# Performance work log

Hardware: AMD Instinct MI355X
Metric: run time of the kernel (lower is better)

Reference implementation:

```python
import jax, jax.numpy as jnp
import numpy as np

N, E, G = 50000, 800000, 128
IN, H, OUT = 64, 108, 108
EPS = 1e-12  # F.normalize eps


def _linear_params(key, fin, fout):
    s = 1.0 / np.sqrt(fin)
    kw, kb = jax.random.split(key)
    W = jax.random.uniform(kw, (fin, fout), jnp.float32, -s, s)
    b = jax.random.uniform(kb, (fout,), jnp.float32, -s, s)
    return W, b


def setup_inputs() -> dict:
    key = jax.random.key(0)
    ks = jax.random.split(key, 12)
    nodes_feat = jax.random.normal(ks[0], (N, IN), jnp.float32)
    edges_feat = jax.random.normal(ks[1], (E, 1), jnp.float32)
    nodes_num_norm_sqrt = jax.random.uniform(ks[2], (N,), jnp.float32)
    edges_num_norm_sqrt = jax.random.uniform(ks[3], (E,), jnp.float32)
    edges_src = jax.random.randint(ks[4], (E,), 0, N, jnp.int32)
    edges_dst = jax.random.randint(ks[5], (E,), 0, N, jnp.int32)
    graph_ids = jnp.sort(jax.random.randint(ks[6], (N,), 0, G, jnp.int32))
    W_emb, b_emb = _linear_params(ks[7], IN, H)
    Wp1, bp1 = _linear_params(ks[8], H, H)      # meanpool MLP, layer 1
    Wn1, bn1 = _linear_params(ks[9], 2 * H, H)  # node-apply, layer 1
    Wp2, bp2 = _linear_params(ks[10], H, H)     # meanpool MLP, output layer
    Wn2, bn2 = _linear_params(ks[11], 2 * H, OUT)
    return dict(nodes_feat=nodes_feat, edges_feat=edges_feat,
                nodes_num_norm_sqrt=nodes_num_norm_sqrt,
                edges_num_norm_sqrt=edges_num_norm_sqrt,
                edges_src=edges_src, edges_dst=edges_dst, graph_ids=graph_ids,
                W_emb=W_emb, b_emb=b_emb, Wp1=Wp1, bp1=bp1, Wn1=Wn1, bn1=bn1,
                Wp2=Wp2, bp2=bp2, Wn2=Wn2, bn2=bn2)


def _sage_layer(h, src, dst, Wp, bp, Wn, bn):
    # GraphSageLayer(meanpool, residual=True, dropout=0): 
    #  m_e = relu(Linear(h_src)); c_v = mean_{e->v} m_e; 
    #  h' = relu(L2norm(Linear([h, c]))); out = h_in + h'
    h_in = h
    m = jax.nn.relu(h @ Wp + bp)                       # pool MLP on nodes, then gather == per-edge MLP
    msg = m[src]                                       # [E, d]
    agg = jax.ops.segment_sum(msg, dst, num_segments=h.shape[0])
    deg = jax.ops.segment_sum(jnp.ones((msg.shape[0],), m.dtype), dst, num_segments=h.shape[0])
    c = agg / jnp.maximum(deg, 1.0)[:, None]           # mean reducer; 0 for isolated nodes
    bundle = jnp.concatenate([h, c], axis=1) @ Wn + bn
    nrm = jnp.linalg.norm(bundle, axis=1, keepdims=True)
    bundle = bundle / jnp.maximum(nrm, EPS)            # F.normalize(p=2, dim=1)
    return h_in + jax.nn.relu(bundle)


def reference(nodes_feat, edges_feat, nodes_num_norm_sqrt, edges_num_norm_sqrt,
              edges_src, edges_dst, graph_ids,
              W_emb, b_emb, Wp1, bp1, Wn1, bn1, Wp2, bp2, Wn2, bn2):
    h = nodes_feat @ W_emb + b_emb                      # embedding_h
    h = _sage_layer(h, edges_src, edges_dst, Wp1, bp1, Wn1, bn1)
    h = _sage_layer(h, edges_src, edges_dst, Wp2, bp2, Wn2, bn2)
    # dgl.mean_nodes: per-graph mean of node features
    s = jax.ops.segment_sum(h, graph_ids, num_segments=G)
    cnt = jax.ops.segment_sum(jnp.ones((h.shape[0],), h.dtype), graph_ids, num_segments=G)
    return s / jnp.maximum(cnt, 1.0)[:, None]           # [G, OUT]
```

## Files before the change

### kernel.cpp

```cpp
#include <hip/hip_runtime.h>

#define N_NODES 50000
#define N_EDGES 800000
#define NG      128
#define FIN     64
#define HD      108
#define SCAN_B  49
#define CNT_B   3125
#define DEGP    16

typedef __attribute__((ext_vector_type(8))) short s16x8;
typedef __attribute__((ext_vector_type(4))) float f32x4;

__device__ __forceinline__ unsigned short bf16_rne(float x) {
    unsigned u = __float_as_uint(x);
    u += 0x7FFFu + ((u >> 16) & 1u);
    return (unsigned short)(u >> 16);
}
__device__ __forceinline__ float bf16_to_f(unsigned u16) {
    return __uint_as_float(u16 << 16);
}

__global__ void prep_k(const float* __restrict__ feat, unsigned short* __restrict__ fbf,
                       unsigned short* __restrict__ hc,
                       const float* __restrict__ W0, const float* __restrict__ W1,
                       const float* __restrict__ W2, const float* __restrict__ W3,
                       const float* __restrict__ W4, unsigned short* __restrict__ Wf,
                       int* __restrict__ deg_p, float* __restrict__ gsum,
                       const int* __restrict__ gids, int* __restrict__ gcnt,
                       int* __restrict__ done) {
    int b = blockIdx.x, t = threadIdx.x;
    if (b < 1563) {
        int i = b * 256 + t;
        if (i < N_NODES * FIN / 8) {
            const float4* p = (const float4*)(feat + (size_t)i * 8);
            float4 a = p[0], c = p[1];
            s16x8 o;
            o[0] = (short)bf16_rne(a.x); o[1] = (short)bf16_rne(a.y);
            o[2] = (short)bf16_rne(a.z); o[3] = (short)bf16_rne(a.w);
            o[4] = (short)bf16_rne(c.x); o[5] = (short)bf16_rne(c.y);
            o[6] = (short)bf16_rne(c.z); o[7] = (short)bf16_rne(c.w);
            *(s16x8*)(fbf + (size_t)i * 8) = o;
        }
    } else if (b < 1759) {
        int i = (b - 1563) * 256 + t;
        if (i < N_NODES) {
            s16x8 z = {0, 0, 0, 0, 0, 0, 0, 0};
            *(s16x8*)(hc + (size_t)i * 224 + 216) = z;
        }
    } else if (b < 1801) {
        int tile = (b - 1759) * 4 + (t >> 6), lane = t & 63;
        if (tile < 168) {
            int kst = tile / 7, nt = tile % 7;
            const float* W; int Kr, ks;
            if (kst < 2)       { W = W0; Kr = 64;  ks = kst;      }
            else if (kst < 6)  { W = W1; Kr = 108; ks = kst - 2;  }
            else if (kst < 13) { W = W2; Kr = 216; ks = kst - 6;  }
            else if (kst < 17) { W = W3; Kr = 108; ks = kst - 13; }
            else               { W = W4; Kr = 216; ks = kst - 17; }
            int n = nt * 16 + (lane & 15);
            s16x8 o;
            #pragma unroll
            for (int j = 0; j < 8; ++j) {
                int k = ks * 32 + (lane >> 4) * 8 + j;
                float v = (k < Kr && n < HD) ? W[k * HD + n] : 0.0f;
                o[j] = (short)bf16_rne(v);
            }
            *(s16x8*)(Wf + (size_t)tile * 512 + lane * 8) = o;
        }
    } else if (b < 2583) {
        int i = (b - 1801) * 256 + t;
        if (i < N_NODES * DEGP / 4) ((int4*)deg_p)[i] = (int4){0, 0, 0, 0};
    } else if (b < 2597) {
        int i = (b - 2583) * 256 + t;
        if (i < NG * HD / 4) ((int4*)gsum)[i] = (int4){0, 0, 0, 0};
        if (b == 2583 && t == 0) *done = 0;
    } else {
        int g = t;
        if (g < NG) {
            int lo = 0, hi = N_NODES;
            while (lo < hi) { int mid = (lo + hi) >> 1; if (gids[mid] < g) lo = mid + 1; else hi = mid; }
            int s = lo;
            lo = s; hi = N_NODES;
            while (lo < hi) { int mid = (lo + hi) >> 1; if (gids[mid] < g + 1) lo = mid + 1; else hi = mid; }
            gcnt[g] = lo - s;
        }
    }
}

__global__ void scan1_k(const int* __restrict__ deg_p, int* __restrict__ rowp,
                        int* __restrict__ bsum, int* __restrict__ boff,
                        int* __restrict__ done) {
    __shared__ int s_w[16];
    __shared__ int s_last;
    int t = threadIdx.x, lane = t & 63, wid = t >> 6;
    int i = blockIdx.x * 1024 + t;
    int v = (i < N_NODES) ? deg_p[(size_t)i * DEGP] : 0;
    int x = v;
    #pragma unroll
    for (int off = 1; off < 64; off <<= 1) {
        int y = __shfl_up(x, off);
        if (lane >= off) x += y;
    }
    if (lane == 63) s_w[wid] = x;
    __syncthreads();
    if (t < 16) {
        int y = s_w[t];
        #pragma unroll
        for (int off = 1; off < 16; off <<= 1) {
            int z = __shfl_up(y, off);
            if (t >= off) y += z;
        }
        s_w[t] = y;
    }
    __syncthreads();
    int woff = wid ? s_w[wid - 1] : 0;
    if (i < N_NODES) rowp[i] = woff + x - v;
    if (t == 1023) {
        bsum[blockIdx.x] = s_w[15];
        __threadfence();
        s_last = (atomicAdd(done, 1) == SCAN_B - 1);
    }
    __syncthreads();
    if (s_last) {
        __threadfence();
        if (t < 64) {
            int v2 = (t < SCAN_B) ? bsum[t] : 0;
            int x2 = v2;
            #pragma unroll
            for (int off = 1; off < 64; off <<= 1) {
                int y2 = __shfl_up(x2, off);
                if (t >= off) x2 += y2;
            }
            if (t < SCAN_B) boff[t] = x2 - v2;
            if (t == SCAN_B - 1) rowp[N_NODES] = x2;
        }
    }
}

__global__ void fill_k(const int* __restrict__ src, const int* __restrict__ dst,
                       const int* __restrict__ rowp, const int* __restrict__ boff,
                       const int* __restrict__ pos, int* __restrict__ csr) {
    int e = blockIdx.x * 256 + threadIdx.x;
    if (e < N_EDGES) {
        int d = dst[e];
        csr[rowp[d] + boff[d >> 10] + pos[e]] = src[e];
    }
}

template <int KSTEPS, int EPI>
__device__ __forceinline__ void gemm_body(
    int blk,
    const unsigned short* __restrict__ A, int strideA,
    const unsigned short* __restrict__ Wf, const float* __restrict__ bias,
    const unsigned short* __restrict__ Wfp, const float* __restrict__ biasp,
    unsigned short* __restrict__ hc, unsigned short* __restrict__ m_out,
    const int* __restrict__ gids, float* __restrict__ gsum) {
    __shared__ unsigned short s_t[4][16][136];
    int t = threadIdx.x, lane = t & 63, wave = t >> 6;
    int wrow = (blk * 4 + wave) * 16;
    if (wrow >= N_NODES) return;
    int l15 = lane & 15, lg = lane >> 4;

    f32x4 acc[7];
    #pragma unroll
    for (int nt = 0; nt < 7; ++nt) acc[nt] = (f32x4){0.f, 0.f, 0.f, 0.f};

    const unsigned short* arow = A + (size_t)(wrow + l15) * strideA + lg * 8;
    #pragma unroll
    for (int ks = 0; ks < KSTEPS; ++ks) {
        s16x8 a = *(const s16x8*)(arow + ks * 32);
        const unsigned short* wp = Wf + ((size_t)(ks * 7) * 64 + lane) * 8;
        #pragma unroll
        for (int nt = 0; nt < 7; ++nt) {
            s16x8 bfr = *(const s16x8*)(wp + (size_t)nt * 512);
            acc[nt] = __builtin_amdgcn_mfma_f32_16x16x32_bf16(a, bfr, acc[nt], 0, 0, 0);
        }
    }

    float vals[7][4];
    if (EPI == 0) {
        #pragma unroll
        for (int nt = 0; nt < 7; ++nt) {
            int col = nt * 16 + l15;
            float bv = (col < HD) ? bias[col] : 0.0f;
            #pragma unroll
            for (int r = 0; r < 4; ++r) vals[nt][r] = acc[nt][r] + bv;
        }
    } else {
        float ss[4] = {0.f, 0.f, 0.f, 0.f};
        #pragma unroll
        for (int nt = 0; nt < 7; ++nt) {
            int col = nt * 16 + l15;
            bool valid = (col < HD);
            float bv = valid ? bias[col] : 0.0f;
            #pragma unroll
            for (int r = 0; r < 4; ++r) {
                float v = valid ? (acc[nt][r] + bv) : 0.0f;
                vals[nt][r] = v;
                ss[r] += v * v;
            }
        }
        #pragma unroll
        for (int r = 0; r < 4; ++r) {
            ss[r] += __shfl_xor(ss[r], 1);
            ss[r] += __shfl_xor(ss[r], 2);
            ss[r] += __shfl_xor(ss[r], 4);
            ss[r] += __shfl_xor(ss[r], 8);
        }
        float rn[4];
        #pragma unroll
        for (int r = 0; r < 4; ++r) rn[r] = 1.0f / fmaxf(sqrtf(ss[r]), 1e-12f);
        #pragma unroll
        for (int nt = 0; nt < 7; ++nt) {
            int col = nt * 16 + l15;
            bool valid = (col < HD);
            #pragma unroll
            for (int r = 0; r < 4; ++r) {
                int row = wrow + lg * 4 + r;
                float hv = valid ? bf16_to_f(hc[(size_t)row * 224 + col]) : 0.0f;
                vals[nt][r] = hv + fmaxf(vals[nt][r] * rn[r], 0.0f);
            }
        }
    }

    if (EPI == 3) {
        int g0 = gids[wrow], g15 = gids[wrow + 15];
        if (g0 == g15) {
            #pragma unroll
            for (int nt = 0; nt < 7; ++nt) {
                int col = nt * 16 + l15;
                float cs = vals[nt][0] + vals[nt][1] + vals[nt][2] + vals[nt][3];
                cs += __shfl_xor(cs, 16);
                cs += __shfl_xor(cs, 32);
                if (lane < 16 && col < HD) atomicAdd(&gsum[g0 * HD + col], cs);
            }
        } else {
            int gr[4];
            #pragma unroll
            for (int r = 0; r < 4; ++r) gr[r] = gids[wrow + lg * 4 + r];
            #pragma unroll
            for (int nt = 0; nt < 7; ++nt) {
                int col = nt * 16 + l15;
                if (col >= HD) continue;
                #pragma unroll
                for (int r = 0; r < 4; ++r)
                    atomicAdd(&gsum[gr[r] * HD + col], vals[nt][r]);
            }
        }
        return;
    }

    #pragma unroll
    for (int nt = 0; nt < 7; ++nt) {
        int col = nt * 16 + l15;
        #pragma unroll
        for (int r = 0; r < 4; ++r) {
            unsigned short hb = (col < HD) ? bf16_rne(vals[nt][r]) : 0;
            s_t[wave][lg * 4 + r][col] = hb;
        }
    }
    #pragma unroll
    for (int p = 0; p < 2; ++p) {
        int idx = p * 64 + lane;
        int row = idx >> 3, q = idx & 7;
        *(unsigned*)&s_t[wave][row][112 + q * 2] = 0u;
    }

    #pragma unroll
    for (int p = 0; p < 4; ++p) {
        int seg = p * 4 + lg;
        if (seg < 14)
            *(s16x8*)(hc + (size_t)(wrow + l15) * 224 + seg * 8) =
                *(const s16x8*)&s_t[wave][l15][seg * 8];
    }

    f32x4 accp[7];
    #pragma unroll
    for (int nt = 0; nt < 7; ++nt) accp[nt] = (f32x4){0.f, 0.f, 0.f, 0.f};
    #pragma unroll
    for (int ks = 0; ks < 4; ++ks) {
        s16x8 a = *(const s16x8*)&s_t[wave][l15][ks * 32 + lg * 8];
        const unsigned short* wp = Wfp + ((size_t)(ks * 7) * 64 + lane) * 8;
        #pragma unroll
        for (int nt = 0; nt < 7; ++nt) {
            s16x8 bfr = *(const s16x8*)(wp + (size_t)nt * 512);
            accp[nt] = __builtin_amdgcn_mfma_f32_16x16x32_bf16(a, bfr, accp[nt], 0, 0, 0);
        }
    }
    #pragma unroll
    for (int nt = 0; nt < 7; ++nt) {
        int col = nt * 16 + l15;
        float bv = (col < HD) ? biasp[col] : 0.0f;
        #pragma unroll
        for (int r = 0; r < 4; ++r)
            s_t[wave][lg * 4 + r][col] = bf16_rne(fmaxf(accp[nt][r] + bv, 0.0f));
    }
    #pragma unroll
    for (int p = 0; p < 4; ++p) {
        int seg = p * 4 + lg;
        if (seg < 14) {
            int ch = seg >> 2, sub = seg & 3;
            *(s16x8*)(m_out + ((size_t)ch * N_NODES + (wrow + l15)) * 32 + sub * 8) =
                *(const s16x8*)&s_t[wave][l15][seg * 8];
        }
    }
}

template <int KSTEPS, int EPI>
__global__ __launch_bounds__(256) void gemm_k(
    const unsigned short* __restrict__ A, int strideA,
    const unsigned short* __restrict__ Wf, const float* __restrict__ bias,
    const unsigned short* __restrict__ Wfp, const float* __restrict__ biasp,
    unsigned short* __restrict__ hc, unsigned short* __restrict__ m_out,
    const int* __restrict__ gids, float* __restrict__ gsum) {
    gemm_body<KSTEPS, EPI>(blockIdx.x, A, strideA, Wf, bias, Wfp, biasp,
                           hc, m_out, gids, gsum);
}

__global__ __launch_bounds__(256) void mix_k(
    const int* __restrict__ dst, int* __restrict__ deg_p, int* __restrict__ pos,
    const unsigned short* __restrict__ fbf,
    const unsigned short* __restrict__ Wf_emb, const float* __restrict__ bemb,
    const unsigned short* __restrict__ Wf_p1, const float* __restrict__ bp1,
    unsigned short* __restrict__ hc, unsigned short* __restrict__ m_out) {
    if (blockIdx.x < CNT_B) {
        int e = blockIdx.x * 256 + threadIdx.x;
        if (e < N_EDGES) pos[e] = atomicAdd(&deg_p[(size_t)dst[e] * DEGP], 1);
    } else {
        gemm_body<2, 0>(blockIdx.x - CNT_B, fbf, FIN, Wf_emb, bemb, Wf_p1, bp1,
                        hc, m_out, nullptr, nullptr);
    }
}

__global__ __launch_bounds__(256) void aggregate_k(
    const unsigned short* __restrict__ m,
    const int* __restrict__ rowp, const int* __restrict__ boff,
    const int* __restrict__ csr, unsigned short* __restrict__ hc) {
    int chunk = blockIdx.x & 3;
    int nblk  = blockIdx.x >> 2;
    int t = threadIdx.x, lane = t & 63, wave = t >> 6;
    int v = nblk * 64 + wave * 16 + (lane >> 2);
    if (v >= N_NODES) return;
    int sub = lane & 3;
    int co = sub * 8;
    int gcol = chunk * 32 + co;
    bool active = (gcol < 112);
    int grp = lane & ~3;
    const unsigned short* mc = m + (size_t)chunk * N_NODES * 32 + co;
    int beg = rowp[v] + boff[v >> 10];
    int end = (v + 1 < N_NODES) ? rowp[v + 1] + boff[(v + 1) >> 10] : rowp[N_NODES];
    float s[8] = {0.f, 0.f, 0.f, 0.f, 0.f, 0.f, 0.f, 0.f};

    int i = beg;
    int p0 = i + sub, p1 = i + 4 + sub;
    int c0 = (p0 < end) ? csr[p0] : -1;
    int c1 = (p1 < end) ? csr[p1] : -1;
    while (i < end) {
        int ni = i + 8;
        int n0 = -1, n1 = -1;
        if (ni < end) {
            int q0 = ni + sub, q1 = ni + 4 + sub;
            n0 = (q0 < end) ? csr[q0] : -1;
            n1 = (q1 < end) ? csr[q1] : -1;
        }
        #pragma unroll
        for (int j = 0; j < 4; ++j) {
            int sv = __shfl(c0, grp + j);
            if (sv >= 0 && active) {
                s16x8 a = *(const s16x8*)(mc + (size_t)sv * 32);
                #pragma unroll
                for (int q = 0; q < 8; ++q) s[q] += bf16_to_f((unsigned short)a[q]);
            }
        }
        #pragma unroll
        for (int j = 0; j < 4; ++j) {
            int sv = __shfl(c1, grp + j);
            if (sv >= 0 && active) {
                s16x8 a = *(const s16x8*)(mc + (size_t)sv * 32);
                #pragma unroll
                for (int q = 0; q < 8; ++q) s[q] += bf16_to_f((unsigned short)a[q]);
            }
        }
        c0 = n0; c1 = n1; i = ni;
    }

    if (active) {
        int degv = end - beg;
        float inv = (degv > 0) ? 1.0f / (float)degv : 0.0f;
        unsigned short* dstp = hc + (size_t)v * 224 + HD + gcol;
        #pragma unroll
        for (int j2 = 0; j2 < 4; ++j2) {
            unsigned pk = (unsigned)bf16_rne(s[2 * j2] * inv) |
                          ((unsigned)bf16_rne(s[2 * j2 + 1] * inv) << 16);
            *(unsigned*)(dstp + 2 * j2) = pk;
        }
    }
}

__global__ void finalize_k(const float* __restrict__ gsum, const int* __restrict__ gcnt,
                           float* __restrict__ out) {
    int i = blockIdx.x * 256 + threadIdx.x;
    if (i < NG * HD) {
        int g = i / HD;
        int cnt = gcnt[g];
        float inv = (cnt > 0) ? 1.0f / (float)cnt : 0.0f;
        out[i] = gsum[i] * inv;
    }
}

extern "C" void kernel_launch(void* const* d_in, const int* in_sizes, int n_in,
                              void* d_out, int out_size, void* d_ws, size_t ws_size,
                              hipStream_t stream) {
    const float* feat = (const float*)d_in[0];
    const int* src  = (const int*)d_in[4];
    const int* dst  = (const int*)d_in[5];
    const int* gids = (const int*)d_in[6];
    const float* Wemb = (const float*)d_in[7];
    const float* bemb = (const float*)d_in[8];
    const float* Wp1  = (const float*)d_in[9];
    const float* bp1  = (const float*)d_in[10];
    const float* Wn1  = (const float*)d_in[11];
    const float* bn1  = (const float*)d_in[12];
    const float* Wp2  = (const float*)d_in[13];
    const float* bp2  = (const float*)d_in[14];
    const float* Wn2  = (const float*)d_in[15];
    const float* bn2  = (const float*)d_in[16];
    float* out = (float*)d_out;
    (void)in_sizes; (void)n_in; (void)out_size; (void)ws_size;

    char* ws = (char*)d_ws;
    size_t off = 0;
    auto carve = [&](size_t bytes) -> char* {
        char* p = ws + off;
        off = (off + bytes + 255) & ~(size_t)255;
        return p;
    };
    unsigned short* hc    = (unsigned short*)carve((size_t)N_NODES * 224 * 2);
    unsigned short* m_bf  = (unsigned short*)carve((size_t)4 * N_NODES * 32 * 2);
    unsigned short* fbf   = (unsigned short*)carve((size_t)N_NODES * FIN * 2);
    unsigned short* Wf    = (unsigned short*)carve((size_t)24 * 7 * 512 * 2);
    int* deg_p = (int*)carve((size_t)N_NODES * DEGP * 4);
    int* rowp  = (int*)carve((size_t)(N_NODES + 1) * 4);
    int* pos   = (int*)carve((size_t)N_EDGES * 4);
    int* csr   = (int*)carve((size_t)N_EDGES * 4);
    int* bsum  = (int*)carve((size_t)SCAN_B * 4);
    int* boff  = (int*)carve((size_t)SCAN_B * 4);
    float* gsum = (float*)carve((size_t)NG * HD * 4);
    int*   gcnt = (int*)carve((size_t)NG * 4);
    int*   done = (int*)carve(4);

    prep_k<<<2598, 256, 0, stream>>>(feat, fbf, hc, Wemb, Wp1, Wn1, Wp2, Wn2, Wf,
                                     deg_p, gsum, gids, gcnt, done);

    const int GB = (N_NODES / 16 + 3) / 4;
    const int AB = 4 * ((N_NODES + 63) / 64);
    unsigned short* Wf_emb = Wf + (size_t)0  * 7 * 512;
    unsigned short* Wf_p1  = Wf + (size_t)2  * 7 * 512;
    unsigned short* Wf_n1  = Wf + (size_t)6  * 7 * 512;
    unsigned short* Wf_p2  = Wf + (size_t)13 * 7 * 512;
    unsigned short* Wf_n2  = Wf + (size_t)17 * 7 * 512;

    mix_k<<<CNT_B + GB, 256, 0, stream>>>(dst, deg_p, pos, fbf, Wf_emb, bemb,
                                          Wf_p1, bp1, hc, m_bf);

    scan1_k<<<SCAN_B, 1024, 0, stream>>>(deg_p, rowp, bsum, boff, done);
    fill_k<<<(N_EDGES + 255) / 256, 256, 0, stream>>>(src, dst, rowp, boff, pos, csr);

    aggregate_k<<<AB, 256, 0, stream>>>(m_bf, rowp, boff, csr, hc);
    gemm_k<7, 2><<<GB, 256, 0, stream>>>(hc, 224, Wf_n1, bn1, Wf_p2, bp2,
                                         hc, m_bf, nullptr, nullptr);
    aggregate_k<<<AB, 256, 0, stream>>>(m_bf, rowp, boff, csr, hc);
    gemm_k<7, 3><<<GB, 256, 0, stream>>>(hc, 224, Wf_n2, bn2, nullptr, nullptr,
                                         hc, nullptr, gids, gsum);

    finalize_k<<<(NG * HD + 255) / 256, 256, 0, stream>>>(gsum, gcnt, out);
}
```

Before: 186.5 us.

## Build CSR with atomic cursors instead of stored per-edge positions

The degree-count pass no longer keeps the atomicAdd return value in a per-edge pos array. The scan now writes a per-node cursor copy of the exclusive offsets, and fill_k claims slots with atomicAdd on that cursor. Both the count and fill kernels now process four edges per thread, with fewer blocks. This removes the 3.2 MB pos write and read, but adds a second round of atomics in fill_k and makes the order of edges within each CSR row nondeterministic, which can change float summation order in aggregation.

```diff
diff --git a/kernel.cpp b/kernel.cpp
--- a/kernel.cpp
+++ b/kernel.cpp
@@ -6,7 +6,7 @@
 #define FIN     64
 #define HD      108
 #define SCAN_B  49
-#define CNT_B   3125
+#define CNT_B   782
 #define DEGP    16
 
 typedef __attribute__((ext_vector_type(8))) short s16x8;
@@ -89,6 +89,7 @@
 }
 
 __global__ void scan1_k(const int* __restrict__ deg_p, int* __restrict__ rowp,
+                        int* __restrict__ cursor,
                         int* __restrict__ bsum, int* __restrict__ boff,
                         int* __restrict__ done) {
     __shared__ int s_w[16];
@@ -115,7 +116,11 @@
     }
     __syncthreads();
     int woff = wid ? s_w[wid - 1] : 0;
-    if (i < N_NODES) rowp[i] = woff + x - v;
+    if (i < N_NODES) {
+        int ex = woff + x - v;
+        rowp[i]   = ex;
+        cursor[i] = ex;
+    }
     if (t == 1023) {
         bsum[blockIdx.x] = s_w[15];
         __threadfence();
@@ -139,12 +144,17 @@
 }
 
 __global__ void fill_k(const int* __restrict__ src, const int* __restrict__ dst,
-                       const int* __restrict__ rowp, const int* __restrict__ boff,
-                       const int* __restrict__ pos, int* __restrict__ csr) {
-    int e = blockIdx.x * 256 + threadIdx.x;
-    if (e < N_EDGES) {
-        int d = dst[e];
-        csr[rowp[d] + boff[d >> 10] + pos[e]] = src[e];
+                       int* __restrict__ cursor, const int* __restrict__ boff,
+                       int* __restrict__ csr) {
+    int e0 = blockIdx.x * 1024 + threadIdx.x;
+    #pragma unroll
+    for (int k = 0; k < 4; ++k) {
+        int e = e0 + k * 256;
+        if (e < N_EDGES) {
+            int d = dst[e];
+            int idx = atomicAdd(&cursor[d], 1) + boff[d >> 10];
+            csr[idx] = src[e];
+        }
     }
 }
 
@@ -319,14 +329,18 @@
 }
 
 __global__ __launch_bounds__(256) void mix_k(
-    const int* __restrict__ dst, int* __restrict__ deg_p, int* __restrict__ pos,
+    const int* __restrict__ dst, int* __restrict__ deg_p,
     const unsigned short* __restrict__ fbf,
     const unsigned short* __restrict__ Wf_emb, const float* __restrict__ bemb,
     const unsigned short* __restrict__ Wf_p1, const float* __restrict__ bp1,
     unsigned short* __restrict__ hc, unsigned short* __restrict__ m_out) {
     if (blockIdx.x < CNT_B) {
-        int e = blockIdx.x * 256 + threadIdx.x;
-        if (e < N_EDGES) pos[e] = atomicAdd(&deg_p[(size_t)dst[e] * DEGP], 1);
+        int e0 = blockIdx.x * 1024 + threadIdx.x;
+        #pragma unroll
+        for (int k = 0; k < 4; ++k) {
+            int e = e0 + k * 256;
+            if (e < N_EDGES) atomicAdd(&deg_p[(size_t)dst[e] * DEGP], 1);
+        }
     } else {
         gemm_body<2, 0>(blockIdx.x - CNT_B, fbf, FIN, Wf_emb, bemb, Wf_p1, bp1,
                         hc, m_out, nullptr, nullptr);
@@ -440,12 +454,12 @@
     unsigned short* m_bf  = (unsigned short*)carve((size_t)4 * N_NODES * 32 * 2);
     unsigned short* fbf   = (unsigned short*)carve((size_t)N_NODES * FIN * 2);
     unsigned short* Wf    = (unsigned short*)carve((size_t)24 * 7 * 512 * 2);
-    int* deg_p = (int*)carve((size_t)N_NODES * DEGP * 4);
-    int* rowp  = (int*)carve((size_t)(N_NODES + 1) * 4);
-    int* pos   = (int*)carve((size_t)N_EDGES * 4);
-    int* csr   = (int*)carve((size_t)N_EDGES * 4);
-    int* bsum  = (int*)carve((size_t)SCAN_B * 4);
-    int* boff  = (int*)carve((size_t)SCAN_B * 4);
+    int* deg_p  = (int*)carve((size_t)N_NODES * DEGP * 4);
+    int* rowp   = (int*)carve((size_t)(N_NODES + 1) * 4);
+    int* cursor = (int*)carve((size_t)N_NODES * 4);
+    int* csr    = (int*)carve((size_t)N_EDGES * 4);
+    int* bsum   = (int*)carve((size_t)SCAN_B * 4);
+    int* boff   = (int*)carve((size_t)SCAN_B * 4);
     float* gsum = (float*)carve((size_t)NG * HD * 4);
     int*   gcnt = (int*)carve((size_t)NG * 4);
     int*   done = (int*)carve(4);
@@ -461,11 +475,11 @@
     unsigned short* Wf_p2  = Wf + (size_t)13 * 7 * 512;
     unsigned short* Wf_n2  = Wf + (size_t)17 * 7 * 512;
 
-    mix_k<<<CNT_B + GB, 256, 0, stream>>>(dst, deg_p, pos, fbf, Wf_emb, bemb,
+    mix_k<<<CNT_B + GB, 256, 0, stream>>>(dst, deg_p, fbf, Wf_emb, bemb,
                                           Wf_p1, bp1, hc, m_bf);
 
-    scan1_k<<<SCAN_B, 1024, 0, stream>>>(deg_p, rowp, bsum, boff, done);
-    fill_k<<<(N_EDGES + 255) / 256, 256, 0, stream>>>(src, dst, rowp, boff, pos, csr);
+    scan1_k<<<SCAN_B, 1024, 0, stream>>>(deg_p, rowp, cursor, bsum, boff, done);
+    fill_k<<<CNT_B, 256, 0, stream>>>(src, dst, cursor, boff, csr);
 
     aggregate_k<<<AB, 256, 0, stream>>>(m_bf, rowp, boff, csr, hc);
     gemm_k<7, 2><<<GB, 256, 0, stream>>>(hc, 224, Wf_n1, bn1, Wf_p2, bp2,
```

Result: slower. 236.3 us (+26.7%).
